# Optimization experiments

Measured on AMD Instinct MI355X. Metric: run time of the kernel, lower is better.

Reference implementation:

```python
import jax, jax.numpy as jnp
import numpy as np

D = 1024   # cfg.hid (downscaled from 8192)
M = 20000  # cfg.mem_c // 2 (downscaled)
B, LQ = 4, 8
PLAST_S = 0.05
IMPORTANCE = 1.0


def mha_shared_kv(q, kv_k, kv_v, Wi, bi, Wo, bo, nheads):
    """torch nn.MultiheadAttention (batch_first) with batch-shared K/V.
    q: [B,Lq,D]; kv_k/kv_v: [Lk,D] shared across batch (avoids the .repeat()
    materialization in the original torch code while computing identical math)."""
    dh = D // nheads
    Wq, Wk, Wv = jnp.split(Wi, 3, axis=0)
    bq, bk, bv = jnp.split(bi, 3)
    qp = (jnp.einsum('bqd,ed->bqe', q, Wq) + bq) * (dh ** -0.5)
    kp = kv_k @ Wk.T + bk              # [Lk,D]
    vp = kv_v @ Wv.T + bv              # [Lk,D]
    qh = qp.reshape(q.shape[0], q.shape[1], nheads, dh)      # [B,Lq,h,dh]
    kh = kp.reshape(kp.shape[0], nheads, dh)                 # [Lk,h,dh]
    vh = vp.reshape(vp.shape[0], nheads, dh)                 # [Lk,h,dh]
    scores = jnp.einsum('bqhd,khd->bhqk', qh, kh)            # [B,h,Lq,Lk]
    attn = jax.nn.softmax(scores, axis=-1)
    ctx = jnp.einsum('bhqk,khd->bqhd', attn, vh)
    ctx = ctx.reshape(q.shape[0], q.shape[1], D)
    return ctx @ Wo.T + bo


def setup_inputs() -> dict:
    key = jax.random.key(0)
    ks = jax.random.split(key, 16)
    s = 0.02
    return {
        'q':    jax.random.normal(ks[0], (B, LQ, D), jnp.float32),
        'data': jax.random.normal(ks[1], (B, D), jnp.float32),
        'ek':   jax.random.normal(ks[2], (M, D), jnp.float32),
        'ev':   jax.random.normal(ks[3], (M, D), jnp.float32),
        'sk':   jax.random.normal(ks[4], (M, D), jnp.float32),
        'sv':   jax.random.normal(ks[5], (M, D), jnp.float32),
        'wm':   jax.random.normal(ks[6], (10, D), jnp.float32),
        'Wi_e': jax.random.normal(ks[7], (3 * D, D), jnp.float32) * s,
        'bi_e': jnp.zeros((3 * D,), jnp.float32),
        'Wo_e': jax.random.normal(ks[8], (D, D), jnp.float32) * s,
        'bo_e': jnp.zeros((D,), jnp.float32),
        'Wi_s': jax.random.normal(ks[9], (3 * D, D), jnp.float32) * s,
        'bi_s': jnp.zeros((3 * D,), jnp.float32),
        'Wo_s': jax.random.normal(ks[10], (D, D), jnp.float32) * s,
        'bo_s': jnp.zeros((D,), jnp.float32),
        'Wi_w': jax.random.normal(ks[11], (3 * D, D), jnp.float32) * s,
        'bi_w': jnp.zeros((3 * D,), jnp.float32),
        'Wo_w': jax.random.normal(ks[12], (D, D), jnp.float32) * s,
        'bo_w': jnp.zeros((D,), jnp.float32),
        'Wrp':  jax.random.normal(ks[13], (D, 3 * D), jnp.float32) * s,
        'brp':  jnp.zeros((D,), jnp.float32),
        'eu':   jnp.zeros((M,), jnp.float32),
    }


def reference(q, data, ek, ev, sk, sv, wm,
              Wi_e, bi_e, Wo_e, bo_e,
              Wi_s, bi_s, Wo_s, bo_s,
              Wi_w, bi_w, Wo_w, bo_w,
              Wrp, brp, eu):
    # ---- NeuroMemory.read ----
    e_r = mha_shared_kv(q, ek, ev, Wi_e, bi_e, Wo_e, bo_e, 16)
    s_r = mha_shared_kv(q, sk, sv, Wi_s, bi_s, Wo_s, bo_s, 16)
    w_r = mha_shared_kv(q, wm, wm, Wi_w, bi_w, Wo_w, bo_w, 8)
    read_out = jnp.concatenate([e_r, s_r, w_r], axis=-1) @ Wrp.T + brp  # [B,Lq,D]

    # ---- NeuroMemory.write (episodic, Hebbian plasticity update) ----
    scores = data @ ek.T                       # [B,M]
    probs = jax.nn.softmax(scores, axis=-1)    # [B,M]
    upd = probs * (PLAST_S * IMPORTANCE)       # [B,M]
    u = upd.mean(axis=0)[:, None]              # [M,1] (batch-mean update strength)
    d = data.mean(axis=0)[None, :]             # [1,D]
    new_ek = ek * (1.0 - u) + d * u            # [M,D]
    new_ev = ev * (1.0 - u) + d * u            # [M,D]
    new_eu = eu * 0.99 + jax.lax.stop_gradient(probs.sum(axis=0))  # [M]
    return (read_out, new_ek, new_ev, new_eu)
```

## Files before the change

### kernel.cpp

```cpp
#include <hip/hip_runtime.h>
#include <hip/hip_fp16.h>
#include <hip/hip_bf16.h>
#include <cstdint>
#include <cstddef>

#define D_HID 1024
#define MEM_M 20000
#define NBATCH 4
#define BL 32
#define NROWS 512
#define SROWS_E 516
#define SROWS_S 512
#define BK 32
#define LDT 40
#define PV_NC 16

typedef __attribute__((ext_vector_type(8))) short short8;
typedef __attribute__((ext_vector_type(4))) float f32x4;
typedef __attribute__((ext_vector_type(4))) unsigned short us4;

__device__ inline ushort f2bf(float f) {
    __hip_bfloat16 b = __float2bfloat16(f);
    return *reinterpret_cast<ushort*>(&b);
}
__device__ inline float h2f(ushort u) {
    __half h; *reinterpret_cast<ushort*>(&h) = u; return __half2float(h);
}

struct SkDesc  { const float* A; const float* B; int K; int M; };
struct SkDescs { SkDesc d[5]; };
struct RdDesc  { const float* bias; float* dst; int M; int ldc; float alpha; };
struct RdDescs { RdDesc d[5]; };

__global__ __launch_bounds__(256)
void k_skinny(SkDescs ds, float* __restrict__ part)
{
    const int g = blockIdx.z;
    const int kc = blockIdx.y, nkc = gridDim.y;
    const int n0 = blockIdx.x * 64;
    const SkDesc dd = ds.d[g];
    const int K = dd.K, M = dd.M;
    const int k0 = kc * 128;

    __shared__ float As[32][132];
    __shared__ float Bs[64][129];
    const int tid = threadIdx.x;
    {
        const int r = tid >> 3, cbl = (tid & 7) * 16;
        if (r < M) {
            const float* src = dd.A + (size_t)r * K + k0 + cbl;
            #pragma unroll
            for (int i = 0; i < 4; ++i) {
                const float4 v = *(const float4*)(src + i * 4);
                As[r][cbl + i * 4 + 0] = v.x; As[r][cbl + i * 4 + 1] = v.y;
                As[r][cbl + i * 4 + 2] = v.z; As[r][cbl + i * 4 + 3] = v.w;
            }
        } else {
            #pragma unroll
            for (int i = 0; i < 16; ++i) As[r][cbl + i] = 0.f;
        }
    }
    {
        const int r = tid >> 2, cbl = (tid & 3) * 32;
        const float* src = dd.B + (size_t)(n0 + r) * K + k0 + cbl;
        #pragma unroll
        for (int i = 0; i < 8; ++i) {
            const float4 v = *(const float4*)(src + i * 4);
            Bs[r][cbl + i * 4 + 0] = v.x; Bs[r][cbl + i * 4 + 1] = v.y;
            Bs[r][cbl + i * 4 + 2] = v.z; Bs[r][cbl + i * 4 + 3] = v.w;
        }
    }
    __syncthreads();
    const int n = tid & 63, mg = tid >> 6;
    float acc[8];
    #pragma unroll
    for (int i = 0; i < 8; ++i) acc[i] = 0.f;
    #pragma unroll 4
    for (int k = 0; k < 128; k += 4) {
        const float b0 = Bs[n][k + 0], b1 = Bs[n][k + 1];
        const float b2 = Bs[n][k + 2], b3 = Bs[n][k + 3];
        #pragma unroll
        for (int i = 0; i < 8; ++i) {
            const float4 a = *(const float4*)&As[mg * 8 + i][k];
            acc[i] = fmaf(a.x, b0, fmaf(a.y, b1, fmaf(a.z, b2, fmaf(a.w, b3, acc[i]))));
        }
    }
    #pragma unroll
    for (int i = 0; i < 8; ++i)
        part[((size_t)(g * nkc + kc) * 32 + mg * 8 + i) * 1024 + n0 + n] = acc[i];
}

__global__ __launch_bounds__(256)
void k_skred(RdDescs ds, const float* __restrict__ part, int nkc)
{
    const int g = blockIdx.y;
    const int m = blockIdx.x;
    const RdDesc dd = ds.d[g];
    if (m >= dd.M) return;
    const int c = threadIdx.x * 4;
    float4 s = make_float4(0.f, 0.f, 0.f, 0.f);
    for (int kc = 0; kc < nkc; ++kc) {
        const float4 v = *(const float4*)&part[((size_t)(g * nkc + kc) * 32 + m) * 1024 + c];
        s.x += v.x; s.y += v.y; s.z += v.z; s.w += v.w;
    }
    const float4 b = *(const float4*)(dd.bias + c);
    float4 o;
    o.x = (s.x + b.x) * dd.alpha; o.y = (s.y + b.y) * dd.alpha;
    o.z = (s.z + b.z) * dd.alpha; o.w = (s.w + b.w) * dd.alpha;
    *(float4*)(dd.dst + (size_t)m * dd.ldc + c) = o;
}

__global__ __launch_bounds__(256)
void mfma_scores(const ushort* __restrict__ A_e, const float* __restrict__ ek,
                 const ushort* __restrict__ A_s, const float* __restrict__ sk,
                 __half* __restrict__ S_e, __half* __restrict__ S_s,
                 const float* __restrict__ c0_e, const float* __restrict__ c0_s)
{
    __shared__ ushort As[2][128][LDT];
    __shared__ ushort Bs[2][128][LDT];
    const int tid = threadIdx.x;
    const int i = blockIdx.x + 9 * blockIdx.y;
    const int xcd = i & 7, idx = i >> 3;
    const int wg = (xcd < 5 ? xcd * 177 : 885 + (xcd - 5) * 176) + idx;
    const int mi = wg % 9, nbk = wg / 9;
    const int bank = (mi >= 5);
    const int m0 = (bank ? (mi - 5) : mi) * 128;
    const int n0 = nbk * 128;
    const ushort* __restrict__ A = bank ? A_s : A_e;
    const float* __restrict__ B = bank ? sk : ek;
    __half* __restrict__ S = bank ? S_s : S_e;
    const float* __restrict__ c0 = bank ? c0_s : c0_e;
    const int Mreal = bank ? SROWS_S : SROWS_E;

    const int wid = tid >> 6, lane = tid & 63;
    const int wr = (wid >> 1) * 64, wc = (wid & 1) * 64;
    const int l15 = lane & 15, l4 = lane >> 4;

    const int srow = tid >> 1;
    const int ac = (tid & 1) * 16;
    int gbrow = n0 + srow; if (gbrow > MEM_M - 1) gbrow = MEM_M - 1;
    const ushort* Ap = A + (size_t)(m0 + srow) * 1024 + ac;
    const float*  Bp = B + (size_t)gbrow * 1024 + ac;

    f32x4 acc[4][4];
    const f32x4 fz = {0.f, 0.f, 0.f, 0.f};
    #pragma unroll
    for (int ii = 0; ii < 4; ++ii)
        #pragma unroll
        for (int j = 0; j < 4; ++j) acc[ii][j] = fz;

    short8 ra0 = *(const short8*)(Ap + 0);
    short8 ra1 = *(const short8*)(Ap + 8);
    float4 rb0 = *(const float4*)(Bp + 0);
    float4 rb1 = *(const float4*)(Bp + 4);
    float4 rb2 = *(const float4*)(Bp + 8);
    float4 rb3 = *(const float4*)(Bp + 12);
    *(short8*)&As[0][srow][ac]     = ra0;
    *(short8*)&As[0][srow][ac + 8] = ra1;
    {
        alignas(16) ushort tb[16];
        tb[0]=f2bf(rb0.x); tb[1]=f2bf(rb0.y); tb[2]=f2bf(rb0.z); tb[3]=f2bf(rb0.w);
        tb[4]=f2bf(rb1.x); tb[5]=f2bf(rb1.y); tb[6]=f2bf(rb1.z); tb[7]=f2bf(rb1.w);
        tb[8]=f2bf(rb2.x); tb[9]=f2bf(rb2.y); tb[10]=f2bf(rb2.z); tb[11]=f2bf(rb2.w);
        tb[12]=f2bf(rb3.x); tb[13]=f2bf(rb3.y); tb[14]=f2bf(rb3.z); tb[15]=f2bf(rb3.w);
        *(short8*)&Bs[0][srow][ac]     = *(short8*)&tb[0];
        *(short8*)&Bs[0][srow][ac + 8] = *(short8*)&tb[8];
    }
    __syncthreads();
    int cur = 0;
    for (int kt = 0; kt < 1024; kt += BK) {
        const bool more = (kt + BK) < 1024;
        if (more) {
            ra0 = *(const short8*)(Ap + kt + BK);
            ra1 = *(const short8*)(Ap + kt + BK + 8);
            rb0 = *(const float4*)(Bp + kt + BK);
            rb1 = *(const float4*)(Bp + kt + BK + 4);
            rb2 = *(const float4*)(Bp + kt + BK + 8);
            rb3 = *(const float4*)(Bp + kt + BK + 12);
        }
        short8 a[4], b[4];
        #pragma unroll
        for (int f = 0; f < 4; ++f) {
            a[f] = *(const short8*)&As[cur][wr + f * 16 + l15][l4 * 8];
            b[f] = *(const short8*)&Bs[cur][wc + f * 16 + l15][l4 * 8];
        }
        #pragma unroll
        for (int ii = 0; ii < 4; ++ii)
            #pragma unroll
            for (int j = 0; j < 4; ++j)
                acc[ii][j] = __builtin_amdgcn_mfma_f32_16x16x32_bf16(a[ii], b[j], acc[ii][j], 0, 0, 0);
        if (more) {
            *(short8*)&As[cur ^ 1][srow][ac]     = ra0;
            *(short8*)&As[cur ^ 1][srow][ac + 8] = ra1;
            alignas(16) ushort tb[16];
            tb[0]=f2bf(rb0.x); tb[1]=f2bf(rb0.y); tb[2]=f2bf(rb0.z); tb[3]=f2bf(rb0.w);
            tb[4]=f2bf(rb1.x); tb[5]=f2bf(rb1.y); tb[6]=f2bf(rb1.z); tb[7]=f2bf(rb1.w);
            tb[8]=f2bf(rb2.x); tb[9]=f2bf(rb2.y); tb[10]=f2bf(rb2.z); tb[11]=f2bf(rb2.w);
            tb[12]=f2bf(rb3.x); tb[13]=f2bf(rb3.y); tb[14]=f2bf(rb3.z); tb[15]=f2bf(rb3.w);
            *(short8*)&Bs[cur ^ 1][srow][ac]     = *(short8*)&tb[0];
            *(short8*)&Bs[cur ^ 1][srow][ac + 8] = *(short8*)&tb[8];
        }
        __syncthreads();
        cur ^= 1;
    }
    #pragma unroll
    for (int ii = 0; ii < 4; ++ii) {
        #pragma unroll
        for (int r = 0; r < 4; ++r) {
            const int row = m0 + wr + ii * 16 + l4 * 4 + r;
            if (row >= Mreal) continue;
            const float cr = c0[row];
            #pragma unroll
            for (int j = 0; j < 4; ++j) {
                const int col = n0 + wc + j * 16 + l15;
                if (col < MEM_M)
                    S[(size_t)row * MEM_M + col] = __float2half(acc[ii][j][r] + cr);
            }
        }
    }
}

__global__ __launch_bounds__(256)
void mfma_pv(const ushort* __restrict__ P_e, const ushort* __restrict__ P_s,
             const float* __restrict__ ev, const float* __restrict__ sv,
             float* __restrict__ part)
{
    __shared__ ushort As[2][128][LDT];
    __shared__ ushort Bs[2][128][LDT];
    const int tid = threadIdx.x;
    const int z = blockIdx.z;
    const int bank = z >> 4, c = z & 15;
    const ushort* __restrict__ P = bank ? P_s : P_e;
    const float* __restrict__ V = bank ? sv : ev;
    const int m0 = blockIdx.y * 128, n0 = blockIdx.x * 128;
    const int ks0 = (c * 625) / PV_NC, ks1 = ((c + 1) * 625) / PV_NC;
    const int wid = tid >> 6, lane = tid & 63;
    const int wr = (wid >> 1) * 64, wc = (wid & 1) * 64;
    const int l15 = lane & 15, l4 = lane >> 4;
    const int kb = (tid & 7) * 4, nb2 = (tid >> 3) * 4;
    const int srow = tid >> 1, ac = (tid & 1) * 16;
    const ushort* Pp = P + (size_t)(m0 + srow) * MEM_M + ac;

    f32x4 acc[4][4];
    const f32x4 fz = {0.f, 0.f, 0.f, 0.f};
    #pragma unroll
    for (int i = 0; i < 4; ++i)
        #pragma unroll
        for (int j = 0; j < 4; ++j) acc[i][j] = fz;

    const int kt0 = ks0 * 32;
    short8 ra0 = *(const short8*)(Pp + kt0);
    short8 ra1 = *(const short8*)(Pp + kt0 + 8);
    float4 rb0 = *(const float4*)(V + (size_t)(kt0 + kb + 0) * 1024 + n0 + nb2);
    float4 rb1 = *(const float4*)(V + (size_t)(kt0 + kb + 1) * 1024 + n0 + nb2);
    float4 rb2 = *(const float4*)(V + (size_t)(kt0 + kb + 2) * 1024 + n0 + nb2);
    float4 rb3 = *(const float4*)(V + (size_t)(kt0 + kb + 3) * 1024 + n0 + nb2);
    *(short8*)&As[0][srow][ac]     = ra0;
    *(short8*)&As[0][srow][ac + 8] = ra1;
    {
        us4 w;
        w.x = f2bf(rb0.x); w.y = f2bf(rb1.x); w.z = f2bf(rb2.x); w.w = f2bf(rb3.x);
        *(us4*)&Bs[0][nb2 + 0][kb] = w;
        w.x = f2bf(rb0.y); w.y = f2bf(rb1.y); w.z = f2bf(rb2.y); w.w = f2bf(rb3.y);
        *(us4*)&Bs[0][nb2 + 1][kb] = w;
        w.x = f2bf(rb0.z); w.y = f2bf(rb1.z); w.z = f2bf(rb2.z); w.w = f2bf(rb3.z);
        *(us4*)&Bs[0][nb2 + 2][kb] = w;
        w.x = f2bf(rb0.w); w.y = f2bf(rb1.w); w.z = f2bf(rb2.w); w.w = f2bf(rb3.w);
        *(us4*)&Bs[0][nb2 + 3][kb] = w;
    }
    __syncthreads();
    int cur = 0;
    for (int ks = ks0; ks < ks1; ++ks) {
        const bool more = (ks + 1) < ks1;
        if (more) {
            const int kt = (ks + 1) * 32;
            ra0 = *(const short8*)(Pp + kt);
            ra1 = *(const short8*)(Pp + kt + 8);
            rb0 = *(const float4*)(V + (size_t)(kt + kb + 0) * 1024 + n0 + nb2);
            rb1 = *(const float4*)(V + (size_t)(kt + kb + 1) * 1024 + n0 + nb2);
            rb2 = *(const float4*)(V + (size_t)(kt + kb + 2) * 1024 + n0 + nb2);
            rb3 = *(const float4*)(V + (size_t)(kt + kb + 3) * 1024 + n0 + nb2);
        }
        short8 a[4], b[4];
        #pragma unroll
        for (int f = 0; f < 4; ++f) {
            a[f] = *(const short8*)&As[cur][wr + f * 16 + l15][l4 * 8];
            b[f] = *(const short8*)&Bs[cur][wc + f * 16 + l15][l4 * 8];
        }
        #pragma unroll
        for (int i = 0; i < 4; ++i)
            #pragma unroll
            for (int j = 0; j < 4; ++j)
                acc[i][j] = __builtin_amdgcn_mfma_f32_16x16x32_bf16(a[i], b[j], acc[i][j], 0, 0, 0);
        if (more) {
            *(short8*)&As[cur ^ 1][srow][ac]     = ra0;
            *(short8*)&As[cur ^ 1][srow][ac + 8] = ra1;
            us4 w;
            w.x = f2bf(rb0.x); w.y = f2bf(rb1.x); w.z = f2bf(rb2.x); w.w = f2bf(rb3.x);
            *(us4*)&Bs[cur ^ 1][nb2 + 0][kb] = w;
            w.x = f2bf(rb0.y); w.y = f2bf(rb1.y); w.z = f2bf(rb2.y); w.w = f2bf(rb3.y);
            *(us4*)&Bs[cur ^ 1][nb2 + 1][kb] = w;
            w.x = f2bf(rb0.z); w.y = f2bf(rb1.z); w.z = f2bf(rb2.z); w.w = f2bf(rb3.z);
            *(us4*)&Bs[cur ^ 1][nb2 + 2][kb] = w;
            w.x = f2bf(rb0.w); w.y = f2bf(rb1.w); w.z = f2bf(rb2.w); w.w = f2bf(rb3.w);
            *(us4*)&Bs[cur ^ 1][nb2 + 3][kb] = w;
        }
        __syncthreads();
        cur ^= 1;
    }
    float* __restrict__ po = part + (size_t)z * NROWS * 1024;
    #pragma unroll
    for (int i = 0; i < 4; ++i)
        #pragma unroll
        for (int r = 0; r < 4; ++r) {
            const int row = m0 + wr + i * 16 + l4 * 4 + r;
            #pragma unroll
            for (int j = 0; j < 4; ++j) {
                const int col = n0 + wc + j * 16 + l15;
                po[(size_t)row * 1024 + col] = acc[i][j][r];
            }
        }
}

__global__ __launch_bounds__(256)
void k_T(const float* __restrict__ qp,
         const float* __restrict__ Wi_e, const float* __restrict__ bi_e,
         const float* __restrict__ Wi_s, const float* __restrict__ bi_s,
         ushort* __restrict__ A_e, float* __restrict__ c0_e,
         ushort* __restrict__ A_s, float* __restrict__ c0_s,
         const float* __restrict__ data, float* __restrict__ dmean)
{
    const int bq = blockIdx.x;
    const int tid = threadIdx.x;
    if (bq >= 128) {
        if (bq < 252) {
            const int row = SROWS_E + (bq - 128);
            us4 z4; z4.x = 0; z4.y = 0; z4.z = 0; z4.w = 0;
            *(us4*)(A_e + (size_t)row * 1024 + tid * 4) = z4;
        } else {
            for (int t = tid; t < D_HID; t += 256) {
                float s = 0.f;
                #pragma unroll
                for (int b = 0; b < NBATCH; ++b) s += data[b * D_HID + t];
                dmean[t] = 0.25f * s;
                #pragma unroll
                for (int b = 0; b < NBATCH; ++b)
                    A_e[(size_t)(NROWS + b) * 1024 + t] = f2bf(data[b * D_HID + t]);
            }
            if (tid < NBATCH) c0_e[NROWS + tid] = 0.f;
        }
        return;
    }
    const int bank = bq >> 6;
    const int h = (bq >> 2) & 15;
    const int q4 = bq & 3;
    const float* qpB = qp + (size_t)bank * BL * D_HID;
    const float* Wk = (bank ? Wi_s : Wi_e) + (size_t)D_HID * D_HID;
    const float* bk = (bank ? bi_s : bi_e) + D_HID;
    ushort* T  = bank ? A_s : A_e;
    float* c0 = bank ? c0_s : c0_e;

    __shared__ float qs[32][64];
    for (int i = tid; i < 32 * 64; i += 256) {
        const int r = i >> 6, j = i & 63;
        qs[r][j] = qpB[(size_t)r * D_HID + h * 64 + j];
    }
    __syncthreads();
    const int e = q4 * 256 + tid;
    float acc[32];
    #pragma unroll
    for (int r = 0; r < 32; ++r) acc[r] = 0.f;
    for (int j = 0; j < 64; ++j) {
        const float w = Wk[(size_t)(h * 64 + j) * D_HID + e];
        #pragma unroll
        for (int r = 0; r < 32; ++r) acc[r] = fmaf(qs[r][j], w, acc[r]);
    }
    #pragma unroll
    for (int r = 0; r < 32; ++r) T[(size_t)(r * 16 + h) * 1024 + e] = f2bf(acc[r]);
    if (q4 == 0 && tid < 32) {
        float s = 0.f;
        for (int j = 0; j < 64; ++j) s += qs[tid][j] * bk[h * 64 + j];
        c0[tid * 16 + h] = s;
    }
}

__global__ __launch_bounds__(256)
void k_softmax(__half* __restrict__ S_e, __half* __restrict__ S_s,
               float* __restrict__ mrow, float* __restrict__ lrow)
{
    const int row = blockIdx.x;
    ushort* p = (row < SROWS_E) ? (ushort*)(S_e + (size_t)row * MEM_M)
                                : (ushort*)(S_s + (size_t)(row - SROWS_E) * MEM_M);
    const bool conv = (row < SROWS_E) ? (row < NROWS) : true;
    __shared__ float red_m[256];
    __shared__ float red_l[256];
    const int tid = threadIdx.x;
    float m = -3.0e38f, l = 0.f;
    for (int c = tid; c < MEM_M / 8; c += 256) {
        alignas(16) ushort t[8];
        *(short8*)t = *(const short8*)(p + c * 8);
        float v[8];
        #pragma unroll
        for (int j = 0; j < 8; ++j) v[j] = h2f(t[j]);
        float cm = v[0];
        #pragma unroll
        for (int j = 1; j < 8; ++j) cm = fmaxf(cm, v[j]);
        const float nm = fmaxf(m, cm);
        float s = 0.f;
        #pragma unroll
        for (int j = 0; j < 8; ++j) s += __expf(v[j] - nm);
        l = l * __expf(m - nm) + s;
        m = nm;
    }
    red_m[tid] = m; red_l[tid] = l; __syncthreads();
    for (int s = 128; s > 0; s >>= 1) {
        if (tid < s) {
            const float m2 = fmaxf(red_m[tid], red_m[tid + s]);
            red_l[tid] = red_l[tid] * __expf(red_m[tid] - m2)
                       + red_l[tid + s] * __expf(red_m[tid + s] - m2);
            red_m[tid] = m2;
        }
        __syncthreads();
    }
    const float rm = red_m[0];
    if (conv) {
        for (int c = tid; c < MEM_M / 8; c += 256) {
            alignas(16) ushort t[8];
            *(short8*)t = *(const short8*)(p + c * 8);
            alignas(16) ushort o[8];
            #pragma unroll
            for (int j = 0; j < 8; ++j) o[j] = f2bf(__expf(h2f(t[j]) - rm));
            *(short8*)(p + c * 8) = *(const short8*)o;
        }
    }
    if (tid == 0) { mrow[row] = rm; lrow[row] = red_l[0]; }
}

__global__ __launch_bounds__(256)
void k_uk(const __half* __restrict__ S_e,
          const float* __restrict__ mrow, const float* __restrict__ lrow,
          const float* __restrict__ eu,
          float* __restrict__ u, float* __restrict__ out_eu)
{
    const int k = blockIdx.x * 256 + threadIdx.x;
    if (k >= MEM_M) return;
    float sp = 0.f;
    #pragma unroll
    for (int b = 0; b < NBATCH; ++b) {
        const int row = NROWS + b;
        sp += __expf(__half2float(S_e[(size_t)row * MEM_M + k]) - mrow[row]) / lrow[row];
    }
    u[k] = 0.05f * 0.25f * sp;
    out_eu[k] = eu[k] * 0.99f + sp;
}

__global__ __launch_bounds__(256)
void k_pvred_upd(const float* __restrict__ part, const float* __restrict__ lrow,
                 float* __restrict__ R,
                 const float* __restrict__ ev, const float* __restrict__ u,
                 const float* __restrict__ dmean, float* __restrict__ out_ev)
{
    const int tid = threadIdx.x;
    if (blockIdx.x < 1024) {
        const size_t perb4 = (size_t)NROWS * 1024 / 4;
        const size_t i = (size_t)blockIdx.x * 256 + tid;
        const int bank = i >= perb4;
        const size_t off4 = i - (size_t)bank * perb4;
        const int m = (int)(off4 >> 8);
        const float inv = 1.f / lrow[bank ? (SROWS_E + m) : m];
        const float4* p = (const float4*)part + (size_t)bank * PV_NC * perb4 + off4;
        float4 s = make_float4(0.f, 0.f, 0.f, 0.f);
        #pragma unroll
        for (int c = 0; c < PV_NC; ++c) {
            const float4 v = p[(size_t)c * perb4];
            s.x += v.x; s.y += v.y; s.z += v.z; s.w += v.w;
        }
        s.x *= inv; s.y *= inv; s.z *= inv; s.w *= inv;
        ((float4*)R)[i] = s;
    } else {
        const int bid = blockIdx.x - 1024;
        const size_t n4 = (size_t)MEM_M * D_HID / 4;
        for (size_t i = (size_t)bid * 256 + tid; i < n4; i += (size_t)1024 * 256) {
            const int k = (int)(i >> 8);
            const int c = (int)(i & 255);
            const float uk = u[k];
            const float om = 1.f - uk;
            const float4 dd = ((const float4*)dmean)[c];
            const float4 b = ((const float4*)ev)[i];
            float4 ob;
            ob.x = b.x * om + dd.x * uk; ob.y = b.y * om + dd.y * uk;
            ob.z = b.z * om + dd.z * uk; ob.w = b.w * om + dd.w * uk;
            ((float4*)out_ev)[i] = ob;
        }
    }
}

__global__ __launch_bounds__(256)
void k_tail(const float* __restrict__ R,
            const float* __restrict__ Wi_e, const float* __restrict__ bi_e,
            const float* __restrict__ Wi_s, const float* __restrict__ bi_s,
            float* __restrict__ ctx,
            const float* __restrict__ qp, const float* __restrict__ kpw,
            const float* __restrict__ vpw,
            const float* __restrict__ ek, const float* __restrict__ u,
            const float* __restrict__ dmean, float* __restrict__ out_ek)
{
    __shared__ float sm[12384];
    const int tid = threadIdx.x;
    const int bx = blockIdx.x;
    if (bx < 32) {
        const int bank = bx >> 4;
        const int h = bx & 15;
        const float* Rb = R + (size_t)bank * NROWS * D_HID;
        const float* Wv = (bank ? Wi_s : Wi_e) + (size_t)2 * D_HID * D_HID;
        const float* bv = (bank ? bi_s : bi_e) + 2 * D_HID;
        float* cb = ctx + (size_t)bank * BL * D_HID;
        float (*Rs)[129] = (float(*)[129])sm;
        float (*Ws)[129] = (float(*)[129])(sm + 32 * 129);
        const int j = tid & 63;
        const int g = tid >> 6;
        float acc[8];
        #pragma unroll
        for (int i = 0; i < 8; ++i) acc[i] = 0.f;
        for (int ec = 0; ec < D_HID; ec += 128) {
            for (int i = tid; i < 32 * 128; i += 256) {
                const int r = i >> 7, e = i & 127;
                Rs[r][e] = Rb[(size_t)(r * 16 + h) * D_HID + ec + e];
            }
            for (int i = tid; i < 64 * 128; i += 256) {
                const int r = i >> 7, e = i & 127;
                Ws[r][e] = Wv[(size_t)(h * 64 + r) * D_HID + ec + e];
            }
            __syncthreads();
            for (int e = 0; e < 128; ++e) {
                const float w = Ws[j][e];
                #pragma unroll
                for (int i = 0; i < 8; ++i)
                    acc[i] = fmaf(Rs[g + 4 * i][e], w, acc[i]);
            }
            __syncthreads();
        }
        #pragma unroll
        for (int i = 0; i < 8; ++i) {
            const int bl = g + 4 * i;
            cb[(size_t)bl * D_HID + h * 64 + j] = acc[i] + bv[h * 64 + j];
        }
    } else if (bx < 64) {
        const int bl = bx - 32;
        float* q = sm;
        float (*kp)[1024] = (float(*)[1024])(sm + 1024);
        float (*pp)[10] = (float(*)[10])(sm + 1024 + 10240);
        const float* qrow = qp + (size_t)(2 * BL + bl) * D_HID;
        for (int i = tid; i < D_HID; i += 256) q[i] = qrow[i];
        for (int i = tid; i < 10 * D_HID; i += 256) kp[i >> 10][i & 1023] = kpw[i];
        __syncthreads();
        if (tid < 80) {
            const int h = tid / 10, k = tid % 10;
            float s = 0.f;
            for (int jj = 0; jj < 128; ++jj) s += q[h * 128 + jj] * kp[k][h * 128 + jj];
            pp[h][k] = s;
        }
        __syncthreads();
        if (tid < 8) {
            float m = -3.0e38f;
            for (int k = 0; k < 10; ++k) m = fmaxf(m, pp[tid][k]);
            float e[10]; float l = 0.f;
            for (int k = 0; k < 10; ++k) { e[k] = __expf(pp[tid][k] - m); l += e[k]; }
            const float inv = 1.f / l;
            for (int k = 0; k < 10; ++k) pp[tid][k] = e[k] * inv;
        }
        __syncthreads();
        float* cw = ctx + (size_t)(2 * BL + bl) * D_HID;
        for (int f = tid; f < D_HID; f += 256) {
            const int h = f >> 7;
            float s = 0.f;
            #pragma unroll
            for (int k = 0; k < 10; ++k) s += pp[h][k] * vpw[(size_t)k * D_HID + f];
            cw[f] = s;
        }
    } else {
        const int bid = bx - 64;
        const size_t n4 = (size_t)MEM_M * D_HID / 4;
        for (size_t i = (size_t)bid * 256 + tid; i < n4; i += (size_t)1024 * 256) {
            const int k = (int)(i >> 8);
            const int c = (int)(i & 255);
            const float uk = u[k];
            const float om = 1.f - uk;
            const float4 dd = ((const float4*)dmean)[c];
            const float4 a = ((const float4*)ek)[i];
            float4 oa;
            oa.x = a.x * om + dd.x * uk; oa.y = a.y * om + dd.y * uk;
            oa.z = a.z * om + dd.z * uk; oa.w = a.w * om + dd.w * uk;
            ((float4*)out_ek)[i] = oa;
        }
    }
}

extern "C" void kernel_launch(void* const* d_in, const int* in_sizes, int n_in,
                              void* d_out, int out_size, void* d_ws, size_t ws_size,
                              hipStream_t stream)
{
    (void)in_sizes; (void)n_in; (void)out_size; (void)ws_size;
    const float* q    = (const float*)d_in[0];
    const float* data = (const float*)d_in[1];
    const float* ek   = (const float*)d_in[2];
    const float* ev   = (const float*)d_in[3];
    const float* sk   = (const float*)d_in[4];
    const float* sv   = (const float*)d_in[5];
    const float* wm   = (const float*)d_in[6];
    const float* Wi_e = (const float*)d_in[7];
    const float* bi_e = (const float*)d_in[8];
    const float* Wo_e = (const float*)d_in[9];
    const float* bo_e = (const float*)d_in[10];
    const float* Wi_s = (const float*)d_in[11];
    const float* bi_s = (const float*)d_in[12];
    const float* Wo_s = (const float*)d_in[13];
    const float* bo_s = (const float*)d_in[14];
    const float* Wi_w = (const float*)d_in[15];
    const float* bi_w = (const float*)d_in[16];
    const float* Wo_w = (const float*)d_in[17];
    const float* bo_w = (const float*)d_in[18];
    const float* Wrp  = (const float*)d_in[19];
    const float* brp  = (const float*)d_in[20];
    const float* eu   = (const float*)d_in[21];

    float* out = (float*)d_out;
    float* out_read = out;
    float* out_ek = out + 32768;
    float* out_ev = out_ek + 20480000;
    float* out_eu = out_ev + 20480000;

    float* ws    = (float*)d_ws;
    float* qp    = ws;
    float* A_e   = qp + 98304;
    float* A_s   = A_e + 655360;
    float* c0_e  = A_s + 524288;
    float* c0_s  = c0_e + 640;
    float* dmean = c0_s + 512;
    float* u     = dmean + 1024;
    float* mrow  = u + 20480;
    float* lrow  = mrow + 1032;
    float* kpw   = lrow + 1032;
    float* vpw   = kpw + 10240;
    float* ctx   = vpw + 10240;
    float* cat   = ctx + 98304;
    float* skpart = cat + 98304;
    float* Rbuf  = skpart;

    ushort* A_e16 = (ushort*)A_e;
    ushort* A_s16 = (ushort*)A_s;

    float* part = out_ek;
    __half* S_e = (__half*)out_ev;
    __half* S_s = S_e + (size_t)SROWS_E * MEM_M;

    const dim3 b256(256);
    const float sc16 = 0.125f;
    const float sc8  = 0.08838834764831845f;

    SkDescs s1;
    s1.d[0] = {q,  Wi_e,            1024, 32};
    s1.d[1] = {q,  Wi_s,            1024, 32};
    s1.d[2] = {q,  Wi_w,            1024, 32};
    s1.d[3] = {wm, Wi_w + 1048576,  1024, 10};
    s1.d[4] = {wm, Wi_w + 2097152,  1024, 10};
    k_skinny<<<dim3(16, 8, 5), b256, 0, stream>>>(s1, skpart);
    RdDescs r1;
    r1.d[0] = {bi_e,        qp,         32, 1024, sc16};
    r1.d[1] = {bi_s,        qp + 32768, 32, 1024, sc16};
    r1.d[2] = {bi_w,        qp + 65536, 32, 1024, sc8};
    r1.d[3] = {bi_w + 1024, kpw,        10, 1024, 1.f};
    r1.d[4] = {bi_w + 2048, vpw,        10, 1024, 1.f};
    k_skred<<<dim3(32, 5), b256, 0, stream>>>(r1, skpart, 8);

    k_T<<<253, b256, 0, stream>>>(qp, Wi_e, bi_e, Wi_s, bi_s,
                                  A_e16, c0_e, A_s16, c0_s, data, dmean);

    mfma_scores<<<dim3(9, 157), b256, 0, stream>>>(A_e16, ek, A_s16, sk, S_e, S_s, c0_e, c0_s);

    k_softmax<<<SROWS_E + SROWS_S, b256, 0, stream>>>(S_e, S_s, mrow, lrow);
    k_uk<<<79, b256, 0, stream>>>(S_e, mrow, lrow, eu, u, out_eu);

    mfma_pv<<<dim3(8, 4, 2 * PV_NC), b256, 0, stream>>>((const ushort*)S_e, (const ushort*)S_s,
                                                        ev, sv, part);

    k_pvred_upd<<<2048, b256, 0, stream>>>(part, lrow, Rbuf, ev, u, dmean, out_ev);

    k_tail<<<1088, b256, 0, stream>>>(Rbuf, Wi_e, bi_e, Wi_s, bi_s, ctx,
                                      qp, kpw, vpw, ek, u, dmean, out_ek);

    SkDescs s2;
    s2.d[0] = {ctx,         Wo_e, 1024, 32};
    s2.d[1] = {ctx + 32768, Wo_s, 1024, 32};
    s2.d[2] = {ctx + 65536, Wo_w, 1024, 32};
    s2.d[3] = {ctx,         Wo_e, 1024, 32};
    s2.d[4] = {ctx,         Wo_e, 1024, 32};
    k_skinny<<<dim3(16, 8, 3), b256, 0, stream>>>(s2, skpart);
    RdDescs r2;
    r2.d[0] = {bo_e, cat,        32, 3072, 1.f};
    r2.d[1] = {bo_s, cat + 1024, 32, 3072, 1.f};
    r2.d[2] = {bo_w, cat + 2048, 32, 3072, 1.f};
    r2.d[3] = r2.d[0];
    r2.d[4] = r2.d[0];
    k_skred<<<dim3(32, 3), b256, 0, stream>>>(r2, skpart, 8);

    SkDescs s3;
    s3.d[0] = {cat, Wrp, 3072, 32};
    s3.d[1] = s3.d[0]; s3.d[2] = s3.d[0]; s3.d[3] = s3.d[0]; s3.d[4] = s3.d[0];
    k_skinny<<<dim3(16, 24, 1), b256, 0, stream>>>(s3, skpart);
    RdDescs r3;
    r3.d[0] = {brp, out_read, 32, 1024, 1.f};
    r3.d[1] = r3.d[0]; r3.d[2] = r3.d[0]; r3.d[3] = r3.d[0]; r3.d[4] = r3.d[0];
    k_skred<<<dim3(32, 1), b256, 0, stream>>>(r3, skpart, 24);

    k_update_done:;
}
```

Measured before the change: 526.1 us.

## Pre-convert ek/sk to bf16 in head kernel and deepen GEMM register prefetch

```diff
diff --git a/kernel.cpp b/kernel.cpp
--- a/kernel.cpp
+++ b/kernel.cpp
@@ -32,19 +32,12 @@
 struct RdDesc  { const float* bias; float* dst; int M; int ldc; float alpha; };
 struct RdDescs { RdDesc d[5]; };
 
-__global__ __launch_bounds__(256)
-void k_skinny(SkDescs ds, float* __restrict__ part)
-{
-    const int g = blockIdx.z;
-    const int kc = blockIdx.y, nkc = gridDim.y;
-    const int n0 = blockIdx.x * 64;
-    const SkDesc dd = ds.d[g];
-    const int K = dd.K, M = dd.M;
-    const int k0 = kc * 128;
-
+__device__ __forceinline__ void skinny_body(const SkDesc dd, float* __restrict__ part,
+                                            int gk, int k0, int n0, int tid)
+{
     __shared__ float As[32][132];
     __shared__ float Bs[64][129];
-    const int tid = threadIdx.x;
+    const int K = dd.K, M = dd.M;
     {
         const int r = tid >> 3, cbl = (tid & 7) * 16;
         if (r < M) {
@@ -87,7 +80,45 @@
     }
     #pragma unroll
     for (int i = 0; i < 8; ++i)
-        part[((size_t)(g * nkc + kc) * 32 + mg * 8 + i) * 1024 + n0 + n] = acc[i];
+        part[((size_t)gk * 32 + mg * 8 + i) * 1024 + n0 + n] = acc[i];
+}
+
+__global__ __launch_bounds__(256)
+void k_skinny(SkDescs ds, float* __restrict__ part)
+{
+    skinny_body(ds.d[blockIdx.z], part,
+                blockIdx.z * gridDim.y + blockIdx.y,
+                blockIdx.y * 128, blockIdx.x * 64, threadIdx.x);
+}
+
+__global__ __launch_bounds__(256)
+void k_head(SkDescs ds, float* __restrict__ part,
+            const float* __restrict__ ek, const float* __restrict__ sk,
+            ushort* __restrict__ kvb)
+{
+    const int bx = blockIdx.x;
+    const int tid = threadIdx.x;
+    if (bx < 640) {
+        const int g = bx >> 7;
+        const int rem = bx & 127;
+        const int kc = rem >> 4;
+        const int n0 = (rem & 15) * 64;
+        skinny_body(ds.d[g], part, g * 8 + kc, kc * 128, n0, tid);
+    } else {
+        const size_t nchunks = (size_t)2 * MEM_M * D_HID / 8;
+        for (size_t i = (size_t)(bx - 640) * 256 + tid; i < nchunks;
+             i += (size_t)1408 * 256) {
+            const size_t base = i * 8;
+            const float* src = (base < (size_t)MEM_M * D_HID)
+                             ? (ek + base) : (sk + base - (size_t)MEM_M * D_HID);
+            const float4 v0 = *(const float4*)(src);
+            const float4 v1 = *(const float4*)(src + 4);
+            alignas(16) ushort o[8];
+            o[0] = f2bf(v0.x); o[1] = f2bf(v0.y); o[2] = f2bf(v0.z); o[3] = f2bf(v0.w);
+            o[4] = f2bf(v1.x); o[5] = f2bf(v1.y); o[6] = f2bf(v1.z); o[7] = f2bf(v1.w);
+            *(short8*)(kvb + base) = *(const short8*)o;
+        }
+    }
 }
 
 __global__ __launch_bounds__(256)
@@ -111,8 +142,8 @@
 }
 
 __global__ __launch_bounds__(256)
-void mfma_scores(const ushort* __restrict__ A_e, const float* __restrict__ ek,
-                 const ushort* __restrict__ A_s, const float* __restrict__ sk,
+void mfma_scores(const ushort* __restrict__ A_e, const ushort* __restrict__ ekb,
+                 const ushort* __restrict__ A_s, const ushort* __restrict__ skb,
                  __half* __restrict__ S_e, __half* __restrict__ S_s,
                  const float* __restrict__ c0_e, const float* __restrict__ c0_s)
 {
@@ -127,7 +158,7 @@
     const int m0 = (bank ? (mi - 5) : mi) * 128;
     const int n0 = nbk * 128;
     const ushort* __restrict__ A = bank ? A_s : A_e;
-    const float* __restrict__ B = bank ? sk : ek;
+    const ushort* __restrict__ B = bank ? skb : ekb;
     __half* __restrict__ S = bank ? S_s : S_e;
     const float* __restrict__ c0 = bank ? c0_s : c0_e;
     const int Mreal = bank ? SROWS_S : SROWS_E;
@@ -140,7 +171,7 @@
     const int ac = (tid & 1) * 16;
     int gbrow = n0 + srow; if (gbrow > MEM_M - 1) gbrow = MEM_M - 1;
     const ushort* Ap = A + (size_t)(m0 + srow) * 1024 + ac;
-    const float*  Bp = B + (size_t)gbrow * 1024 + ac;
+    const ushort* Bp = B + (size_t)gbrow * 1024 + ac;
 
     f32x4 acc[4][4];
     const f32x4 fz = {0.f, 0.f, 0.f, 0.f};
@@ -149,60 +180,52 @@
         #pragma unroll
         for (int j = 0; j < 4; ++j) acc[ii][j] = fz;
 
-    short8 ra0 = *(const short8*)(Ap + 0);
-    short8 ra1 = *(const short8*)(Ap + 8);
-    float4 rb0 = *(const float4*)(Bp + 0);
-    float4 rb1 = *(const float4*)(Bp + 4);
-    float4 rb2 = *(const float4*)(Bp + 8);
-    float4 rb3 = *(const float4*)(Bp + 12);
-    *(short8*)&As[0][srow][ac]     = ra0;
-    *(short8*)&As[0][srow][ac + 8] = ra1;
-    {
-        alignas(16) ushort tb[16];
-        tb[0]=f2bf(rb0.x); tb[1]=f2bf(rb0.y); tb[2]=f2bf(rb0.z); tb[3]=f2bf(rb0.w);
-        tb[4]=f2bf(rb1.x); tb[5]=f2bf(rb1.y); tb[6]=f2bf(rb1.z); tb[7]=f2bf(rb1.w);
-        tb[8]=f2bf(rb2.x); tb[9]=f2bf(rb2.y); tb[10]=f2bf(rb2.z); tb[11]=f2bf(rb2.w);
-        tb[12]=f2bf(rb3.x); tb[13]=f2bf(rb3.y); tb[14]=f2bf(rb3.z); tb[15]=f2bf(rb3.w);
-        *(short8*)&Bs[0][srow][ac]     = *(short8*)&tb[0];
-        *(short8*)&Bs[0][srow][ac + 8] = *(short8*)&tb[8];
-    }
-    __syncthreads();
-    int cur = 0;
-    for (int kt = 0; kt < 1024; kt += BK) {
-        const bool more = (kt + BK) < 1024;
-        if (more) {
-            ra0 = *(const short8*)(Ap + kt + BK);
-            ra1 = *(const short8*)(Ap + kt + BK + 8);
-            rb0 = *(const float4*)(Bp + kt + BK);
-            rb1 = *(const float4*)(Bp + kt + BK + 4);
-            rb2 = *(const float4*)(Bp + kt + BK + 8);
-            rb3 = *(const float4*)(Bp + kt + BK + 12);
-        }
+    auto MF = [&](int bu) {
         short8 a[4], b[4];
         #pragma unroll
         for (int f = 0; f < 4; ++f) {
-            a[f] = *(const short8*)&As[cur][wr + f * 16 + l15][l4 * 8];
-            b[f] = *(const short8*)&Bs[cur][wc + f * 16 + l15][l4 * 8];
+            a[f] = *(const short8*)&As[bu][wr + f * 16 + l15][l4 * 8];
+            b[f] = *(const short8*)&Bs[bu][wc + f * 16 + l15][l4 * 8];
         }
         #pragma unroll
         for (int ii = 0; ii < 4; ++ii)
             #pragma unroll
             for (int j = 0; j < 4; ++j)
                 acc[ii][j] = __builtin_amdgcn_mfma_f32_16x16x32_bf16(a[ii], b[j], acc[ii][j], 0, 0, 0);
-        if (more) {
-            *(short8*)&As[cur ^ 1][srow][ac]     = ra0;
-            *(short8*)&As[cur ^ 1][srow][ac + 8] = ra1;
-            alignas(16) ushort tb[16];
-            tb[0]=f2bf(rb0.x); tb[1]=f2bf(rb0.y); tb[2]=f2bf(rb0.z); tb[3]=f2bf(rb0.w);
-            tb[4]=f2bf(rb1.x); tb[5]=f2bf(rb1.y); tb[6]=f2bf(rb1.z); tb[7]=f2bf(rb1.w);
-            tb[8]=f2bf(rb2.x); tb[9]=f2bf(rb2.y); tb[10]=f2bf(rb2.z); tb[11]=f2bf(rb2.w);
-            tb[12]=f2bf(rb3.x); tb[13]=f2bf(rb3.y); tb[14]=f2bf(rb3.z); tb[15]=f2bf(rb3.w);
-            *(short8*)&Bs[cur ^ 1][srow][ac]     = *(short8*)&tb[0];
-            *(short8*)&Bs[cur ^ 1][srow][ac + 8] = *(short8*)&tb[8];
-        }
+    };
+
+    short8 a00, a01, b00, b01;
+    short8 a10, a11, b10, b11;
+
+#define SC_LOAD0(KT) { a00 = *(const short8*)(Ap + (KT)); a01 = *(const short8*)(Ap + (KT) + 8); \
+                       b00 = *(const short8*)(Bp + (KT)); b01 = *(const short8*)(Bp + (KT) + 8); }
+#define SC_LOAD1(KT) { a10 = *(const short8*)(Ap + (KT)); a11 = *(const short8*)(Ap + (KT) + 8); \
+                       b10 = *(const short8*)(Bp + (KT)); b11 = *(const short8*)(Bp + (KT) + 8); }
+#define SC_STORE0(BU) { *(short8*)&As[BU][srow][ac] = a00; *(short8*)&As[BU][srow][ac + 8] = a01; \
+                        *(short8*)&Bs[BU][srow][ac] = b00; *(short8*)&Bs[BU][srow][ac + 8] = b01; }
+#define SC_STORE1(BU) { *(short8*)&As[BU][srow][ac] = a10; *(short8*)&As[BU][srow][ac + 8] = a11; \
+                        *(short8*)&Bs[BU][srow][ac] = b10; *(short8*)&Bs[BU][srow][ac + 8] = b11; }
+
+    SC_LOAD0(0);
+    SC_LOAD1(32);
+    SC_STORE0(0);
+    __syncthreads();
+    for (int it = 0; it < 16; ++it) {
+        const int kt = it * 64;
+        if (it < 15) SC_LOAD0(kt + 64);
+        MF(0);
+        SC_STORE1(1);
         __syncthreads();
-        cur ^= 1;
-    }
+        if (it < 15) SC_LOAD1(kt + 96);
+        MF(1);
+        if (it < 15) SC_STORE0(0);
+        __syncthreads();
+    }
+#undef SC_LOAD0
+#undef SC_LOAD1
+#undef SC_STORE0
+#undef SC_STORE1
+
     #pragma unroll
     for (int ii = 0; ii < 4; ++ii) {
         #pragma unroll
@@ -240,6 +263,7 @@
     const int kb = (tid & 7) * 4, nb2 = (tid >> 3) * 4;
     const int srow = tid >> 1, ac = (tid & 1) * 16;
     const ushort* Pp = P + (size_t)(m0 + srow) * MEM_M + ac;
+    const float*  Vp = V + (size_t)n0 + nb2;
 
     f32x4 acc[4][4];
     const f32x4 fz = {0.f, 0.f, 0.f, 0.f};
@@ -248,66 +272,79 @@
         #pragma unroll
         for (int j = 0; j < 4; ++j) acc[i][j] = fz;
 
-    const int kt0 = ks0 * 32;
-    short8 ra0 = *(const short8*)(Pp + kt0);
-    short8 ra1 = *(const short8*)(Pp + kt0 + 8);
-    float4 rb0 = *(const float4*)(V + (size_t)(kt0 + kb + 0) * 1024 + n0 + nb2);
-    float4 rb1 = *(const float4*)(V + (size_t)(kt0 + kb + 1) * 1024 + n0 + nb2);
-    float4 rb2 = *(const float4*)(V + (size_t)(kt0 + kb + 2) * 1024 + n0 + nb2);
-    float4 rb3 = *(const float4*)(V + (size_t)(kt0 + kb + 3) * 1024 + n0 + nb2);
-    *(short8*)&As[0][srow][ac]     = ra0;
-    *(short8*)&As[0][srow][ac + 8] = ra1;
-    {
-        us4 w;
-        w.x = f2bf(rb0.x); w.y = f2bf(rb1.x); w.z = f2bf(rb2.x); w.w = f2bf(rb3.x);
-        *(us4*)&Bs[0][nb2 + 0][kb] = w;
-        w.x = f2bf(rb0.y); w.y = f2bf(rb1.y); w.z = f2bf(rb2.y); w.w = f2bf(rb3.y);
-        *(us4*)&Bs[0][nb2 + 1][kb] = w;
-        w.x = f2bf(rb0.z); w.y = f2bf(rb1.z); w.z = f2bf(rb2.z); w.w = f2bf(rb3.z);
-        *(us4*)&Bs[0][nb2 + 2][kb] = w;
-        w.x = f2bf(rb0.w); w.y = f2bf(rb1.w); w.z = f2bf(rb2.w); w.w = f2bf(rb3.w);
-        *(us4*)&Bs[0][nb2 + 3][kb] = w;
-    }
-    __syncthreads();
-    int cur = 0;
-    for (int ks = ks0; ks < ks1; ++ks) {
-        const bool more = (ks + 1) < ks1;
-        if (more) {
-            const int kt = (ks + 1) * 32;
-            ra0 = *(const short8*)(Pp + kt);
-            ra1 = *(const short8*)(Pp + kt + 8);
-            rb0 = *(const float4*)(V + (size_t)(kt + kb + 0) * 1024 + n0 + nb2);
-            rb1 = *(const float4*)(V + (size_t)(kt + kb + 1) * 1024 + n0 + nb2);
-            rb2 = *(const float4*)(V + (size_t)(kt + kb + 2) * 1024 + n0 + nb2);
-            rb3 = *(const float4*)(V + (size_t)(kt + kb + 3) * 1024 + n0 + nb2);
-        }
+    auto MF = [&](int bu) {
         short8 a[4], b[4];
         #pragma unroll
         for (int f = 0; f < 4; ++f) {
-            a[f] = *(const short8*)&As[cur][wr + f * 16 + l15][l4 * 8];
-            b[f] = *(const short8*)&Bs[cur][wc + f * 16 + l15][l4 * 8];
+            a[f] = *(const short8*)&As[bu][wr + f * 16 + l15][l4 * 8];
+            b[f] = *(const short8*)&Bs[bu][wc + f * 16 + l15][l4 * 8];
         }
         #pragma unroll
         for (int i = 0; i < 4; ++i)
             #pragma unroll
             for (int j = 0; j < 4; ++j)
                 acc[i][j] = __builtin_amdgcn_mfma_f32_16x16x32_bf16(a[i], b[j], acc[i][j], 0, 0, 0);
-        if (more) {
-            *(short8*)&As[cur ^ 1][srow][ac]     = ra0;
-            *(short8*)&As[cur ^ 1][srow][ac + 8] = ra1;
-            us4 w;
-            w.x = f2bf(rb0.x); w.y = f2bf(rb1.x); w.z = f2bf(rb2.x); w.w = f2bf(rb3.x);
-            *(us4*)&Bs[cur ^ 1][nb2 + 0][kb] = w;
-            w.x = f2bf(rb0.y); w.y = f2bf(rb1.y); w.z = f2bf(rb2.y); w.w = f2bf(rb3.y);
-            *(us4*)&Bs[cur ^ 1][nb2 + 1][kb] = w;
-            w.x = f2bf(rb0.z); w.y = f2bf(rb1.z); w.z = f2bf(rb2.z); w.w = f2bf(rb3.z);
-            *(us4*)&Bs[cur ^ 1][nb2 + 2][kb] = w;
-            w.x = f2bf(rb0.w); w.y = f2bf(rb1.w); w.z = f2bf(rb2.w); w.w = f2bf(rb3.w);
-            *(us4*)&Bs[cur ^ 1][nb2 + 3][kb] = w;
-        }
+    };
+
+    short8 pa00, pa01, pa10, pa11;
+    float4 q00, q01, q02, q03, q10, q11, q12, q13;
+
+#define PV_LOAD0(T) { const int kt = (T) * 32; \
+    pa00 = *(const short8*)(Pp + kt); pa01 = *(const short8*)(Pp + kt + 8); \
+    q00 = *(const float4*)(Vp + (size_t)(kt + kb + 0) * 1024); \
+    q01 = *(const float4*)(Vp + (size_t)(kt + kb + 1) * 1024); \
+    q02 = *(const float4*)(Vp + (size_t)(kt + kb + 2) * 1024); \
+    q03 = *(const float4*)(Vp + (size_t)(kt + kb + 3) * 1024); }
+#define PV_LOAD1(T) { const int kt = (T) * 32; \
+    pa10 = *(const short8*)(Pp + kt); pa11 = *(const short8*)(Pp + kt + 8); \
+    q10 = *(const float4*)(Vp + (size_t)(kt + kb + 0) * 1024); \
+    q11 = *(const float4*)(Vp + (size_t)(kt + kb + 1) * 1024); \
+    q12 = *(const float4*)(Vp + (size_t)(kt + kb + 2) * 1024); \
+    q13 = *(const float4*)(Vp + (size_t)(kt + kb + 3) * 1024); }
+#define PV_STORE0(BU) { \
+    *(short8*)&As[BU][srow][ac] = pa00; *(short8*)&As[BU][srow][ac + 8] = pa01; \
+    us4 w; \
+    w.x = f2bf(q00.x); w.y = f2bf(q01.x); w.z = f2bf(q02.x); w.w = f2bf(q03.x); \
+    *(us4*)&Bs[BU][nb2 + 0][kb] = w; \
+    w.x = f2bf(q00.y); w.y = f2bf(q01.y); w.z = f2bf(q02.y); w.w = f2bf(q03.y); \
+    *(us4*)&Bs[BU][nb2 + 1][kb] = w; \
+    w.x = f2bf(q00.z); w.y = f2bf(q01.z); w.z = f2bf(q02.z); w.w = f2bf(q03.z); \
+    *(us4*)&Bs[BU][nb2 + 2][kb] = w; \
+    w.x = f2bf(q00.w); w.y = f2bf(q01.w); w.z = f2bf(q02.w); w.w = f2bf(q03.w); \
+    *(us4*)&Bs[BU][nb2 + 3][kb] = w; }
+#define PV_STORE1(BU) { \
+    *(short8*)&As[BU][srow][ac] = pa10; *(short8*)&As[BU][srow][ac + 8] = pa11; \
+    us4 w; \
+    w.x = f2bf(q10.x); w.y = f2bf(q11.x); w.z = f2bf(q12.x); w.w = f2bf(q13.x); \
+    *(us4*)&Bs[BU][nb2 + 0][kb] = w; \
+    w.x = f2bf(q10.y); w.y = f2bf(q11.y); w.z = f2bf(q12.y); w.w = f2bf(q13.y); \
+    *(us4*)&Bs[BU][nb2 + 1][kb] = w; \
+    w.x = f2bf(q10.z); w.y = f2bf(q11.z); w.z = f2bf(q12.z); w.w = f2bf(q13.z); \
+    *(us4*)&Bs[BU][nb2 + 2][kb] = w; \
+    w.x = f2bf(q10.w); w.y = f2bf(q11.w); w.z = f2bf(q12.w); w.w = f2bf(q13.w); \
+    *(us4*)&Bs[BU][nb2 + 3][kb] = w; }
+
+    PV_LOAD0(ks0);
+    if (ks0 + 1 < ks1) PV_LOAD1(ks0 + 1);
+    PV_STORE0(0);
+    __syncthreads();
+    for (int t = ks0; t < ks1; t += 2) {
+        if (t + 2 < ks1) PV_LOAD0(t + 2);
+        MF(0);
+        if (t + 1 < ks1) PV_STORE1(1);
         __syncthreads();
-        cur ^= 1;
-    }
+        if (t + 1 < ks1) {
+            if (t + 3 < ks1) PV_LOAD1(t + 3);
+            MF(1);
+            if (t + 2 < ks1) PV_STORE0(0);
+            __syncthreads();
+        }
+    }
+#undef PV_LOAD0
+#undef PV_LOAD1
+#undef PV_STORE0
+#undef PV_STORE1
+
     float* __restrict__ po = part + (size_t)z * NROWS * 1024;
     #pragma unroll
     for (int i = 0; i < 4; ++i)
@@ -650,6 +687,8 @@
     ushort* A_e16 = (ushort*)A_e;
     ushort* A_s16 = (ushort*)A_s;
 
+    ushort* ekb = (ushort*)out_ek;
+    ushort* skb = ekb + (size_t)MEM_M * D_HID;
     float* part = out_ek;
     __half* S_e = (__half*)out_ev;
     __half* S_s = S_e + (size_t)SROWS_E * MEM_M;
@@ -664,7 +703,7 @@
     s1.d[2] = {q,  Wi_w,            1024, 32};
     s1.d[3] = {wm, Wi_w + 1048576,  1024, 10};
     s1.d[4] = {wm, Wi_w + 2097152,  1024, 10};
-    k_skinny<<<dim3(16, 8, 5), b256, 0, stream>>>(s1, skpart);
+    k_head<<<2048, b256, 0, stream>>>(s1, skpart, ek, sk, ekb);
     RdDescs r1;
     r1.d[0] = {bi_e,        qp,         32, 1024, sc16};
     r1.d[1] = {bi_s,        qp + 32768, 32, 1024, sc16};
@@ -676,7 +715,8 @@
     k_T<<<253, b256, 0, stream>>>(qp, Wi_e, bi_e, Wi_s, bi_s,
                                   A_e16, c0_e, A_s16, c0_s, data, dmean);
 
-    mfma_scores<<<dim3(9, 157), b256, 0, stream>>>(A_e16, ek, A_s16, sk, S_e, S_s, c0_e, c0_s);
+    mfma_scores<<<dim3(9, 157), b256, 0, stream>>>(A_e16, ekb, A_s16, skb,
+                                                   S_e, S_s, c0_e, c0_s);
 
     k_softmax<<<SROWS_E + SROWS_S, b256, 0, stream>>>(S_e, S_s, mrow, lrow);
     k_uk<<<79, b256, 0, stream>>>(S_e, mrow, lrow, eu, u, out_eu);
@@ -712,6 +752,4 @@
     r3.d[0] = {brp, out_read, 32, 1024, 1.f};
     r3.d[1] = r3.d[0]; r3.d[2] = r3.d[0]; r3.d[3] = r3.d[0]; r3.d[4] = r3.d[0];
     k_skred<<<dim3(32, 1), b256, 0, stream>>>(r3, skpart, 24);
-
-    k_update_done:;
-}
+}
```

New measurement: 498.4 us. 1.06x faster.
